# Performance work log

Hardware: AMD Instinct MI355X
Metric: run time of the kernel (lower is better)

Reference implementation:

```python
import jax, jax.numpy as jnp
import numpy as np

BIG = 1.0e9   # sentinel for masked distances / masked max
K_NBR = 64    # max_num_neighbors in radius()


def _fps(pos, n_sample):
    """Farthest point sampling on a single cloud pos [N, D] -> int32 [n_sample]."""
    n = pos.shape[0]

    def body(i, st):
        d, idxs = st
        last = pos[idxs[i - 1]]                              # [D]
        d = jnp.minimum(d, jnp.sum((pos - last) ** 2, axis=-1))
        return d, idxs.at[i].set(jnp.argmax(d).astype(jnp.int32))

    d0 = jnp.full((n,), BIG, pos.dtype)
    idxs0 = jnp.zeros((n_sample,), jnp.int32)
    _, idxs = jax.lax.fori_loop(1, n_sample, body, (d0, idxs0))
    return idxs


def _mlp2(h, w1, b1, w2, b2):
    # PyG MLP([a,b,c]) in eval mode (dropout off, batch-norm at default running
    # stats == identity): Linear -> ReLU -> Linear (plain last layer).
    return jax.nn.relu(h @ w1 + b1) @ w2 + b2


_gather = jax.vmap(lambda a, i: a[i])  # per-cloud fancy gather


def _sa(x, pos, ratio, r, w1, b1, w2, b2):
    """SAModule: FPS -> radius neighbors (<=K) -> PointConv (gather, MLP on
    [x_j, pos_j - pos_i], max-aggregate). Dense batched: x [B,N,C], pos [B,N,D]."""
    B, N, D = pos.shape
    M = int(round(N * ratio))
    idx = jax.vmap(lambda p: _fps(p, M))(pos)                 # [B, M]
    pos_q = _gather(pos, idx)                                 # [B, M, D]
    # pairwise squared distances query -> all points  [B, M, N]
    d2 = jnp.sum((pos_q[:, :, None, :] - pos[:, None, :, :]) ** 2, axis=-1)
    neg = jnp.where(d2 <= r * r, -d2, -BIG)
    vals, nbr = jax.lax.top_k(neg, K_NBR)                     # [B, M, K]
    valid = vals > -0.5 * BIG                                 # in-radius mask
    x_j = _gather(x, nbr)                                     # [B, M, K, C]
    rel = _gather(pos, nbr) - pos_q[:, :, None, :]            # [B, M, K, D]
    h = _mlp2(jnp.concatenate([x_j, rel], axis=-1), w1, b1, w2, b2)
    h = jnp.where(valid[..., None], h, -BIG)
    return jnp.max(h, axis=2), pos_q                          # max aggregation


def setup_inputs() -> dict:
    key = jax.random.key(0)
    ks = jax.random.split(key, 12)
    B, N, D, F = 8, 4096, 2, 5

    def lin(k, fi, fo):
        return (jax.random.normal(k, (fi, fo), jnp.float32) / np.sqrt(fi)).astype(jnp.float32)

    return {
        "x": jax.random.normal(ks[0], (B, N, F), jnp.float32),
        "pos": jax.random.uniform(ks[1], (B, N, D), jnp.float32),
        # sa1: MLP([5+2, 32, 64])
        "w1a": lin(ks[2], 7, 32),   "b1a": jnp.zeros((32,), jnp.float32),
        "w1b": lin(ks[3], 32, 64),  "b1b": jnp.zeros((64,), jnp.float32),
        # sa2: MLP([64+2, 64, 128])
        "w2a": lin(ks[4], 66, 64),  "b2a": jnp.zeros((64,), jnp.float32),
        "w2b": lin(ks[5], 64, 128), "b2b": jnp.zeros((128,), jnp.float32),
        # sa3 (global): MLP([128+2, 128, 256])
        "w3a": lin(ks[6], 130, 128), "b3a": jnp.zeros((128,), jnp.float32),
        "w3b": lin(ks[7], 128, 256), "b3b": jnp.zeros((256,), jnp.float32),
        # head: MLP([256, 256, 1024], norm=None)
        "w4a": lin(ks[8], 256, 256),  "b4a": jnp.zeros((256,), jnp.float32),
        "w4b": lin(ks[9], 256, 1024), "b4b": jnp.zeros((1024,), jnp.float32),
    }


def reference(x, pos, w1a, b1a, w1b, b1b, w2a, b2a, w2b, b2b,
              w3a, b3a, w3b, b3b, w4a, b4a, w4b, b4b):
    h1, p1 = _sa(x, pos, 0.5, 0.2, w1a, b1a, w1b, b1b)       # [B, N/2, 64]
    h2, p2 = _sa(h1, p1, 0.25, 0.4, w2a, b2a, w2b, b2b)      # [B, N/8, 128]
    g = _mlp2(jnp.concatenate([h2, p2], axis=-1), w3a, b3a, w3b, b3b)
    g = jnp.max(g, axis=1)                                    # global max pool [B, 256]
    return _mlp2(g, w4a, b4a, w4b, b4b)                       # [B, 1024]
```

## Files before the change

kernel.cpp:

```cpp
#include <hip/hip_runtime.h>
#include <hip/hip_cooperative_groups.h>

namespace cg = cooperative_groups;


#define DPP_UMAX(u, ctrl)                                                      \
  do {                                                                         \
    unsigned _o = (unsigned)__builtin_amdgcn_update_dpp(0, (int)(u), (ctrl),   \
                                                        0xf, 0xf, true);       \
    (u) = ((u) > _o) ? (u) : _o;                                               \
  } while (0)

template<int PPT, int T>
__device__ __forceinline__ void fps_stage(
    float (&xr)[PPT], float (&yr)[PPT], int Msel, int t,
    const float* srcx, const float* srcy,
    float* outx, float* outy,
    unsigned long long* sp ) {
  constexpr int NW = T / 64;
  constexpr int HP = PPT / 2;
  float lx = srcx[0], ly = srcy[0];
  if (t == 0) { outx[0] = lx; outy[0] = ly; }
  float d[PPT];
#pragma unroll
  for (int k = 0; k < PPT; ++k) d[k] = 1e9f;

  for (int i = 1; i < Msel; ++i) {
#pragma unroll
    for (int k = 0; k < PPT; ++k) {
      float dx = xr[k] - lx, dy = yr[k] - ly;
      float dd = __fadd_rn(__fmul_rn(dx, dx), __fmul_rn(dy, dy));
      d[k] = fminf(d[k], dd);
    }
    float bvA = d[0]; int bkA = 0;
    float bvB = d[HP]; int bkB = HP;
#pragma unroll
    for (int k = 1; k < HP; ++k) {
      if (d[k] > bvA)      { bvA = d[k];      bkA = k; }
      if (d[HP + k] > bvB) { bvB = d[HP + k]; bkB = HP + k; }
    }
    float bv = bvA; int bk = bkA;
    if (bvB > bvA) { bv = bvB; bk = bkB; }
    const int bp = t * PPT + bk;
    const unsigned mybits = __float_as_uint(bv);
    unsigned u = mybits;
    DPP_UMAX(u, 0x111);
    DPP_UMAX(u, 0x112);
    DPP_UMAX(u, 0x114);
    DPP_UMAX(u, 0x118);
    DPP_UMAX(u, 0x142);
    DPP_UMAX(u, 0x143);
    const unsigned wvb = (unsigned)__builtin_amdgcn_readlane((int)u, 63);
    const unsigned long long tmask = __ballot(mybits == wvb);
    const int fl = (int)__builtin_ctzll(tmask);
    const int wbp = __builtin_amdgcn_readlane(bp, fl);
    const int par = i & 1;
    if ((t & 63) == 0)
      sp[par * NW + (t >> 6)] =
          ((unsigned long long)wvb << 32) | (unsigned)(~wbp);
    __syncthreads();
    const unsigned long long* sl = &sp[par * NW];
    unsigned long long best = sl[0];
#pragma unroll
    for (int j = 1; j < NW; ++j) {
      unsigned long long v = sl[j];
      best = (v > best) ? v : best;
    }
    const int wi = (int)(~(unsigned)best);
    lx = srcx[wi]; ly = srcy[wi];
    if (t == 0) { outx[i] = lx; outy[i] = ly; }
  }
}

__global__ __launch_bounds__(512) void mega_kernel(
    const float* __restrict__ pos,
    const float* __restrict__ xin,
    float* __restrict__ posq1,
    float* __restrict__ posq2,
    float* __restrict__ h1,
    const float* __restrict__ W1, const float* __restrict__ B1,
    const float* __restrict__ W2, const float* __restrict__ B2)
{
  constexpr int N = 4096, M1 = 2048, M2 = 512, T = 512;
  constexpr int PPT = N / T, PPT2 = M1 / T, NW = T / 64;
  constexpr int H = 32, CI2 = 7, HS = 36, W1P = 8;
  __shared__ union {
    struct {
      float sx[N], sy[N];
      float wlx[M1], wly[M1];
      float wl2x[M2], wl2y[M2];
      unsigned long long sp[2 * NW];
    } f;
    struct {
      float sW1t[H * W1P];
      float sB1[H];
      float sHH[8 * 64 * HS];
      int   sNbr[8][64];
    } c;
  } sh;
  const int bid = blockIdx.x, t = threadIdx.x;
  cg::grid_group grid = cg::this_grid();

  float xr[PPT], yr[PPT];
  if (bid < 8) {
    const int b = bid;
    const float4* p4 =
        (const float4*)(pos + (size_t)b * N * 2 + (size_t)t * PPT * 2);
#pragma unroll
    for (int q = 0; q < PPT / 2; ++q) {
      float4 v = p4[q];
      xr[2 * q + 0] = v.x; yr[2 * q + 0] = v.y;
      xr[2 * q + 1] = v.z; yr[2 * q + 1] = v.w;
    }
#pragma unroll
    for (int k = 0; k < PPT; ++k) {
      int pt = t * PPT + k;
      sh.f.sx[pt] = xr[k]; sh.f.sy[pt] = yr[k];
    }
    __syncthreads();
    fps_stage<PPT, T>(xr, yr, M1, t, sh.f.sx, sh.f.sy, sh.f.wlx, sh.f.wly,
                      sh.f.sp);
    __syncthreads();
    for (int j = t; j < M1; j += T)
      ((float2*)posq1)[(size_t)b * M1 + j] =
          make_float2(sh.f.wlx[j], sh.f.wly[j]);
    __threadfence();
  }
  grid.sync();

  if (bid < 8) {
    const int b = bid;
    float x2[PPT2], y2[PPT2];
#pragma unroll
    for (int k = 0; k < PPT2; ++k) {
      x2[k] = sh.f.wlx[t * PPT2 + k];
      y2[k] = sh.f.wly[t * PPT2 + k];
    }
    fps_stage<PPT2, T>(x2, y2, M2, t, sh.f.wlx, sh.f.wly, sh.f.wl2x, sh.f.wl2y,
                       sh.f.sp);
    __syncthreads();
    for (int j = t; j < M2; j += T)
      ((float2*)posq2)[(size_t)b * M2 + j] =
          make_float2(sh.f.wl2x[j], sh.f.wl2y[j]);
  } else {
    for (int j = t; j < CI2 * H; j += T) {
      int cc = j / H, hh = j - cc * H;
      sh.c.sW1t[hh * W1P + cc] = W1[j];
    }
    for (int j = t; j < H; j += T) sh.c.sB1[j] = B1[j];
    __syncthreads();
    const int wv = t >> 6, lane = t & 63;
    const unsigned long long below = (1ULL << lane) - 1ULL;
    float* hbase = &sh.c.sHH[wv * 64 * HS];
    int* snb = sh.c.sNbr[wv];
    for (int wid = (bid - 8) * 8 + wv; wid < 16384; wid += 248 * 8) {
      const int b = wid >> 11;
      const float qx = posq1[2 * wid + 0], qy = posq1[2 * wid + 1];
      const float* p = pos + (size_t)b * N * 2;
      snb[lane] = -1;
      unsigned bits[64];
      int cnt = 0;
#pragma unroll
      for (int k = 0; k < 64; ++k) {
        int pt = lane + (k << 6);
        float dx = p[pt * 2 + 0] - qx, dy = p[pt * 2 + 1] - qy;
        float dd = __fadd_rn(__fmul_rn(dx, dx), __fmul_rn(dy, dy));
        bool inr = (dd <= 0.04f);
        bits[k] = inr ? __float_as_uint(dd) : 0xFFFFFFFFu;
        cnt += __popcll(__ballot(inr));
      }
      if (cnt <= 64) {
        int base = 0;
#pragma unroll
        for (int k = 0; k < 64; ++k) {
          bool s = (bits[k] != 0xFFFFFFFFu);
          unsigned long long m = __ballot(s);
          if (s) snb[base + __popcll(m & below)] = lane + (k << 6);
          base += __popcll(m);
        }
      } else {
        unsigned lo = 0, hi = __float_as_uint(0.04f);
        while (lo < hi) {
          unsigned mid = lo + ((hi - lo) >> 1);
          int c = 0;
#pragma unroll
          for (int k = 0; k < 64; ++k) c += __popcll(__ballot(bits[k] <= mid));
          if (c >= 64) hi = mid; else lo = mid + 1;
        }
        int cless = 0;
#pragma unroll
        for (int k = 0; k < 64; ++k) cless += __popcll(__ballot(bits[k] < lo));
        const int need = 64 - cless;
        int base = 0, tiecnt = 0;
#pragma unroll
        for (int k = 0; k < 64; ++k) {
          bool tie = (bits[k] == lo);
          unsigned long long tm = __ballot(tie);
          bool s = (bits[k] < lo) ||
                   (tie && (tiecnt + __popcll(tm & below)) < need);
          tiecnt += __popcll(tm);
          unsigned long long m = __ballot(s);
          if (s) snb[base + __popcll(m & below)] = lane + (k << 6);
          base += __popcll(m);
        }
      }
      const int idx = snb[lane];
      const unsigned long long vm = __ballot(idx >= 0);
      const int ii = (idx < 0) ? 0 : idx;
      float in[CI2];
      {
        const float* xp = xin + ((size_t)b * N + ii) * 5;
#pragma unroll
        for (int c = 0; c < 5; ++c) in[c] = xp[c];
        const float* pp = p + (size_t)ii * 2;
        in[5] = pp[0] - qx;
        in[6] = pp[1] - qy;
      }
#pragma unroll
      for (int h = 0; h < H; h += 4) {
        float vv[4];
#pragma unroll
        for (int j = 0; j < 4; ++j) {
          float a = sh.c.sB1[h + j];
#pragma unroll
          for (int c = 0; c < CI2; ++c)
            a = fmaf(in[c], sh.c.sW1t[(h + j) * W1P + c], a);
          vv[j] = fmaxf(a, 0.0f);
        }
        *(float4*)&hbase[lane * HS + h] = make_float4(vv[0], vv[1], vv[2], vv[3]);
      }
      const int o = lane;
      float w2r[H];
#pragma unroll
      for (int h = 0; h < H; ++h) w2r[h] = W2[h * 64 + o];
      const float b2o = B2[o];
      float m = -1e30f;
      for (int n = 0; n < 64; ++n) {
        const float4* hp = (const float4*)&hbase[n * HS];
        float a = b2o;
#pragma unroll
        for (int j = 0; j < H / 4; ++j) {
          float4 hv = hp[j];
          a = fmaf(hv.x, w2r[4 * j + 0], a);
          a = fmaf(hv.y, w2r[4 * j + 1], a);
          a = fmaf(hv.z, w2r[4 * j + 2], a);
          a = fmaf(hv.w, w2r[4 * j + 3], a);
        }
        a = ((vm >> n) & 1ULL) ? a : -1e9f;
        m = fmaxf(m, a);
      }
      h1[(size_t)wid * 64 + o] = m;
    }
  }
}

template<int CPL>
__global__ __launch_bounds__(256) void nbr_kernel(
    const float* __restrict__ pts, const float* __restrict__ posq,
    int* __restrict__ nbr, int M, int NPTS, int total_q, float R2) {
  const int wid = blockIdx.x * 4 + (threadIdx.x >> 6);
  if (wid >= total_q) return;
  const int lane = threadIdx.x & 63;
  const int b = wid / M;
  const float qx = posq[(size_t)wid * 2 + 0], qy = posq[(size_t)wid * 2 + 1];
  const float* p = pts + (size_t)b * NPTS * 2;
  unsigned bits[CPL];
  int cnt = 0;
#pragma unroll
  for (int k = 0; k < CPL; ++k) {
    int pt = lane + (k << 6);
    float dx = p[pt * 2 + 0] - qx, dy = p[pt * 2 + 1] - qy;
    float dd = __fadd_rn(__fmul_rn(dx, dx), __fmul_rn(dy, dy));
    bool inr = (dd <= R2);
    bits[k] = inr ? __float_as_uint(dd) : 0xFFFFFFFFu;
    cnt += __popcll(__ballot(inr));
  }
  const unsigned long long below = (1ULL << lane) - 1ULL;
  if (cnt <= 64) {
    int base = 0;
#pragma unroll
    for (int k = 0; k < CPL; ++k) {
      bool s = (bits[k] != 0xFFFFFFFFu);
      unsigned long long m = __ballot(s);
      if (s) nbr[(size_t)wid * 64 + base + __popcll(m & below)] = lane + (k << 6);
      base += __popcll(m);
    }
    for (int j = base + lane; j < 64; j += 64) nbr[(size_t)wid * 64 + j] = -1;
  } else {
    unsigned lo = 0, hi = __float_as_uint(R2);
    while (lo < hi) {
      unsigned mid = lo + ((hi - lo) >> 1);
      int c = 0;
#pragma unroll
      for (int k = 0; k < CPL; ++k) c += __popcll(__ballot(bits[k] <= mid));
      if (c >= 64) hi = mid; else lo = mid + 1;
    }
    int cless = 0;
#pragma unroll
    for (int k = 0; k < CPL; ++k) cless += __popcll(__ballot(bits[k] < lo));
    const int need = 64 - cless;
    int base = 0, tiecnt = 0;
#pragma unroll
    for (int k = 0; k < CPL; ++k) {
      bool tie = (bits[k] == lo);
      unsigned long long tm = __ballot(tie);
      bool s = (bits[k] < lo) || (tie && (tiecnt + __popcll(tm & below)) < need);
      tiecnt += __popcll(tm);
      unsigned long long m = __ballot(s);
      if (s) nbr[(size_t)wid * 64 + base + __popcll(m & below)] = lane + (k << 6);
      base += __popcll(m);
    }
  }
}

template<int CIN, int H, int COUT, int QPB, int NPTS, int HS, int W1P>
__global__ __launch_bounds__(64 * QPB) void conv_kernel(
    const float* __restrict__ x, const float* __restrict__ pts,
    const float* __restrict__ posq, const int* __restrict__ nbr,
    const float* __restrict__ W1, const float* __restrict__ b1,
    const float* __restrict__ W2, const float* __restrict__ b2,
    float* __restrict__ out, int M) {
  constexpr int CI2 = CIN + 2;
  __shared__ float sW1t[H * W1P];
  __shared__ float sB1[H];
  __shared__ float sHH[QPB * 64 * HS];
  const int tid = threadIdx.x;
  for (int j = tid; j < CI2 * H; j += 64 * QPB) {
    int c = j / H, h = j - c * H;
    sW1t[h * W1P + c] = W1[j];
  }
  for (int j = tid; j < H; j += 64 * QPB) sB1[j] = b1[j];
  __syncthreads();
  const int wv = tid >> 6, lane = tid & 63;
  const int wid = blockIdx.x * QPB + wv;
  const int b = wid / M;
  const int idx = nbr[(size_t)wid * 64 + lane];
  const unsigned long long vm = __ballot(idx >= 0);
  const int ii = (idx < 0) ? 0 : idx;
  float in[CI2];
  {
    const float* xp = x + ((size_t)b * NPTS + ii) * CIN;
#pragma unroll
    for (int c = 0; c < CIN; ++c) in[c] = xp[c];
    float qx = posq[(size_t)wid * 2 + 0], qy = posq[(size_t)wid * 2 + 1];
    const float* pp = pts + ((size_t)b * NPTS + ii) * 2;
    in[CIN] = pp[0] - qx;
    in[CIN + 1] = pp[1] - qy;
  }
  float* hbase = &sHH[wv * 64 * HS];
#pragma unroll
  for (int h = 0; h < H; h += 4) {
    float vv[4];
#pragma unroll
    for (int j = 0; j < 4; ++j) {
      float a = sB1[h + j];
#pragma unroll
      for (int c = 0; c < CI2; ++c) a = fmaf(in[c], sW1t[(h + j) * W1P + c], a);
      vv[j] = fmaxf(a, 0.0f);
    }
    *(float4*)&hbase[lane * HS + h] = make_float4(vv[0], vv[1], vv[2], vv[3]);
  }
#pragma unroll
  for (int half = 0; half < COUT / 64; ++half) {
    const int o = half * 64 + lane;
    float w2r[H];
#pragma unroll
    for (int h = 0; h < H; ++h) w2r[h] = W2[h * COUT + o];
    const float b2o = b2[o];
    float m = -1e30f;
    for (int n = 0; n < 64; ++n) {
      const float4* hp = (const float4*)&hbase[n * HS];
      float a = b2o;
#pragma unroll
      for (int j = 0; j < H / 4; ++j) {
        float4 hv = hp[j];
        a = fmaf(hv.x, w2r[4 * j + 0], a);
        a = fmaf(hv.y, w2r[4 * j + 1], a);
        a = fmaf(hv.z, w2r[4 * j + 2], a);
        a = fmaf(hv.w, w2r[4 * j + 3], a);
      }
      a = ((vm >> n) & 1ULL) ? a : -1e9f;
      m = fmaxf(m, a);
    }
    out[(size_t)wid * COUT + o] = m;
  }
}

__global__ __launch_bounds__(256) void u_kernel(
    const float* __restrict__ h2, const float* __restrict__ posq2,
    const float* __restrict__ W3a, const float* __restrict__ b3a,
    float* __restrict__ u) {
  const int p = blockIdx.x * 2 + (threadIdx.x >> 7);
  const int h = threadIdx.x & 127;
  const float* hp = h2 + (size_t)p * 128;
  float a = b3a[h];
  for (int c = 0; c < 128; ++c) a = fmaf(hp[c], W3a[c * 128 + h], a);
  a = fmaf(posq2[(size_t)p * 2 + 0], W3a[128 * 128 + h], a);
  a = fmaf(posq2[(size_t)p * 2 + 1], W3a[129 * 128 + h], a);
  u[(size_t)p * 128 + h] = fmaxf(a, 0.0f);
}

__global__ __launch_bounds__(256) void g_kernel(
    const float* __restrict__ u, const float* __restrict__ W3b,
    const float* __restrict__ b3b, float* __restrict__ part) {
  __shared__ float su[64 * 128];
  const int bb = blockIdx.x;
  const float* up = u + (size_t)bb * 64 * 128;
  for (int j = threadIdx.x; j < 64 * 128; j += 256) su[j] = up[j];
  __syncthreads();
  const int o = threadIdx.x;
  float w[128];
#pragma unroll
  for (int h = 0; h < 128; ++h) w[h] = W3b[h * 256 + o];
  float m = -1e30f;
  for (int p = 0; p < 64; ++p) {
    float a = b3b[o];
    const float4* sp = (const float4*)&su[p * 128];
#pragma unroll
    for (int j = 0; j < 32; ++j) {
      float4 v = sp[j];
      a = fmaf(v.x, w[4 * j + 0], a);
      a = fmaf(v.y, w[4 * j + 1], a);
      a = fmaf(v.z, w[4 * j + 2], a);
      a = fmaf(v.w, w[4 * j + 3], a);
    }
    m = fmaxf(m, a);
  }
  part[(size_t)bb * 256 + o] = m;
}

__global__ __launch_bounds__(256) void head_kernel(
    const float* __restrict__ part, const float* __restrict__ W4a,
    const float* __restrict__ b4a, const float* __restrict__ W4b,
    const float* __restrict__ b4b, float* __restrict__ out) {
  __shared__ float g[256], h4[256];
  const int b = blockIdx.x, t = threadIdx.x;
  float m = part[(size_t)(b * 8 + 0) * 256 + t];
  for (int c = 1; c < 8; ++c) m = fmaxf(m, part[(size_t)(b * 8 + c) * 256 + t]);
  g[t] = m;
  __syncthreads();
  float a = b4a[t];
  for (int c = 0; c < 256; ++c) a = fmaf(g[c], W4a[c * 256 + t], a);
  h4[t] = fmaxf(a, 0.0f);
  __syncthreads();
  for (int jj = 0; jj < 4; ++jj) {
    int o = t + jj * 256;
    float a2 = b4b[o];
    for (int c = 0; c < 256; ++c) a2 = fmaf(h4[c], W4b[c * 1024 + o], a2);
    out[(size_t)b * 1024 + o] = a2;
  }
}

extern "C" void kernel_launch(void* const* d_in, const int* in_sizes, int n_in,
                              void* d_out, int out_size, void* d_ws, size_t ws_size,
                              hipStream_t stream) {
  (void)in_sizes; (void)n_in; (void)out_size; (void)ws_size;
  const float* x   = (const float*)d_in[0];
  const float* pos = (const float*)d_in[1];
  const float* w1a = (const float*)d_in[2];  const float* b1a = (const float*)d_in[3];
  const float* w1b = (const float*)d_in[4];  const float* b1b = (const float*)d_in[5];
  const float* w2a = (const float*)d_in[6];  const float* b2a = (const float*)d_in[7];
  const float* w2b = (const float*)d_in[8];  const float* b2b = (const float*)d_in[9];
  const float* w3a = (const float*)d_in[10]; const float* b3a = (const float*)d_in[11];
  const float* w3b = (const float*)d_in[12]; const float* b3b = (const float*)d_in[13];
  const float* w4a = (const float*)d_in[14]; const float* b4a = (const float*)d_in[15];
  const float* w4b = (const float*)d_in[16]; const float* b4b = (const float*)d_in[17];
  float* outp = (float*)d_out;

  char* ws = (char*)d_ws;
  size_t off = 0;
  float* posq1 = (float*)(ws + off); off += (size_t)8 * 2048 * 2 * 4;
  float* posq2 = (float*)(ws + off); off += (size_t)8 * 512 * 2 * 4;
  int*   nbr2  = (int*)  (ws + off); off += (size_t)4096 * 64 * 4;
  float* h1    = (float*)(ws + off); off += (size_t)16384 * 64 * 4;
  float* h2    = (float*)(ws + off); off += (size_t)4096 * 128 * 4;
  float* u3    = (float*)(ws + off); off += (size_t)4096 * 128 * 4;
  float* part  = (float*)(ws + off); off += (size_t)64 * 256 * 4;

  void* kargs[] = {(void*)&pos, (void*)&x, (void*)&posq1, (void*)&posq2,
                   (void*)&h1, (void*)&w1a, (void*)&b1a, (void*)&w1b,
                   (void*)&b1b};
  hipLaunchCooperativeKernel((void*)mega_kernel, dim3(256), dim3(512), kargs,
                             0, stream);
  nbr_kernel<32><<<dim3(1024), dim3(256), 0, stream>>>(posq1, posq2, nbr2,
                                                       512, 2048, 4096, 0.16f);
  conv_kernel<64, 64, 128, 2, 2048, 68, 68><<<dim3(2048), dim3(128), 0, stream>>>(
      h1, posq1, posq2, nbr2, w2a, b2a, w2b, b2b, h2, 512);
  u_kernel<<<dim3(2048), dim3(256), 0, stream>>>(h2, posq2, w3a, b3a, u3);
  g_kernel<<<dim3(64), dim3(256), 0, stream>>>(u3, w3b, b3b, part);
  head_kernel<<<dim3(8), dim3(256), 0, stream>>>(part, w4a, b4a, w4b, b4b, outp);
}
```

Measured before the change: 2.001 ms.

## Stream FPS results to overlap SA1 conv and fuse all stages into one cooperative kernel

The first FPS stage now publishes sampled points to global memory in chunks of 64, each followed by a per-cloud progress counter. The SA1 conv blocks spin on that counter, so they can start before FPS finishes instead of waiting on a grid barrier. The SA2 neighbor search and conv, the SA3 MLP with global max, and the head MLP all move into the same cooperative kernel, separated by grid syncs. This removes five extra kernel launches and the nbr2/u3 intermediate buffers. It also folds W2 register loads out of the per-query loop and adds a launch_bounds occupancy hint of one block. The risks are spin-wait overhead, correctness of the acquire/release fences, and later stages running on only 256 blocks at low occupancy.

```diff
diff --git a/kernel.cpp b/kernel.cpp
--- a/kernel.cpp
+++ b/kernel.cpp
@@ -11,16 +11,18 @@
     (u) = ((u) > _o) ? (u) : _o;                                               \
   } while (0)
 
-template<int PPT, int T>
+template<int PPT, int T, bool PUB>
 __device__ __forceinline__ void fps_stage(
     float (&xr)[PPT], float (&yr)[PPT], int Msel, int t,
     const float* srcx, const float* srcy,
     float* outx, float* outy,
-    unsigned long long* sp ) {
+    unsigned long long* sp ,
+    float2* pq1g, unsigned* prog) {
   constexpr int NW = T / 64;
   constexpr int HP = PPT / 2;
   float lx = srcx[0], ly = srcy[0];
   if (t == 0) { outx[0] = lx; outy[0] = ly; }
+  float px = lx, py = ly;
   float d[PPT];
 #pragma unroll
   for (int k = 0; k < PPT; ++k) d[k] = 1e9f;
@@ -69,41 +71,73 @@
     const int wi = (int)(~(unsigned)best);
     lx = srcx[wi]; ly = srcy[wi];
     if (t == 0) { outx[i] = lx; outy[i] = ly; }
+    if constexpr (PUB) {
+      if ((t >> 6) == NW - 1) {
+        const int lj = t & 63;
+        if (lj == (i & 63)) { px = lx; py = ly; }
+        if ((i & 63) == 63) {
+          pq1g[(i - 63) + lj] = make_float2(px, py);
+          __builtin_amdgcn_fence(__ATOMIC_RELEASE, "agent");
+          if (lj == 0)
+            __hip_atomic_store(prog, (unsigned)(i + 1), __ATOMIC_RELAXED,
+                               __HIP_MEMORY_SCOPE_AGENT);
+        }
+      }
+    }
   }
 }
 
-__global__ __launch_bounds__(512) void mega_kernel(
+union SharedU {
+  struct {
+    float sx[4096], sy[4096];
+    float wlx[2048], wly[2048];
+    float wl2x[512], wl2y[512];
+    unsigned long long sp[16];
+  } f;
+  struct {
+    float sW1t[32 * 8]; float sB1[32];
+    float sHH[8 * 64 * 36]; int sNbr[8][64];
+  } c1;
+  struct {
+    float sW1t[64 * 68]; float sB1[64];
+    float sHH[8 * 64 * 68]; int sNbr[8][64];
+  } c2;
+  struct { float su[16 * 128]; } g;
+  struct { float gg[256]; float h4[256]; } h;
+};
+
+__global__ __launch_bounds__(512, 1) void mega_kernel(
     const float* __restrict__ pos,
     const float* __restrict__ xin,
     float* __restrict__ posq1,
     float* __restrict__ posq2,
     float* __restrict__ h1,
-    const float* __restrict__ W1, const float* __restrict__ B1,
-    const float* __restrict__ W2, const float* __restrict__ B2)
-{
+    float* __restrict__ h2,
+    float* __restrict__ part,
+    unsigned* __restrict__ prog,
+    const float* __restrict__ w1a, const float* __restrict__ b1a,
+    const float* __restrict__ w1b, const float* __restrict__ b1b,
+    const float* __restrict__ w2a, const float* __restrict__ b2a,
+    const float* __restrict__ w2b, const float* __restrict__ b2b,
+    const float* __restrict__ w3a, const float* __restrict__ b3a,
+    const float* __restrict__ w3b, const float* __restrict__ b3b,
+    const float* __restrict__ w4a, const float* __restrict__ b4a,
+    const float* __restrict__ w4b, const float* __restrict__ b4b,
+    float* __restrict__ outp) {
   constexpr int N = 4096, M1 = 2048, M2 = 512, T = 512;
-  constexpr int PPT = N / T, PPT2 = M1 / T, NW = T / 64;
-  constexpr int H = 32, CI2 = 7, HS = 36, W1P = 8;
-  __shared__ union {
-    struct {
-      float sx[N], sy[N];
-      float wlx[M1], wly[M1];
-      float wl2x[M2], wl2y[M2];
-      unsigned long long sp[2 * NW];
-    } f;
-    struct {
-      float sW1t[H * W1P];
-      float sB1[H];
-      float sHH[8 * 64 * HS];
-      int   sNbr[8][64];
-    } c;
-  } sh;
+  constexpr int PPT = N / T, PPT2 = M1 / T;
+  __shared__ SharedU sh;
   const int bid = blockIdx.x, t = threadIdx.x;
   cg::grid_group grid = cg::this_grid();
 
-  float xr[PPT], yr[PPT];
+  if (bid < 8 && t == 0)
+    __hip_atomic_store(&prog[bid], 0u, __ATOMIC_RELAXED,
+                       __HIP_MEMORY_SCOPE_AGENT);
+  grid.sync();
+
   if (bid < 8) {
     const int b = bid;
+    float xr[PPT], yr[PPT];
     const float4* p4 =
         (const float4*)(pos + (size_t)b * N * 2 + (size_t)t * PPT * 2);
 #pragma unroll
@@ -118,44 +152,49 @@
       sh.f.sx[pt] = xr[k]; sh.f.sy[pt] = yr[k];
     }
     __syncthreads();
-    fps_stage<PPT, T>(xr, yr, M1, t, sh.f.sx, sh.f.sy, sh.f.wlx, sh.f.wly,
-                      sh.f.sp);
-    __syncthreads();
-    for (int j = t; j < M1; j += T)
-      ((float2*)posq1)[(size_t)b * M1 + j] =
-          make_float2(sh.f.wlx[j], sh.f.wly[j]);
-    __threadfence();
-  }
-  grid.sync();
-
-  if (bid < 8) {
-    const int b = bid;
+    fps_stage<PPT, T, true>(xr, yr, M1, t, sh.f.sx, sh.f.sy, sh.f.wlx,
+                            sh.f.wly, sh.f.sp,
+                            (float2*)posq1 + (size_t)b * M1, &prog[b]);
+    __syncthreads();
     float x2[PPT2], y2[PPT2];
 #pragma unroll
     for (int k = 0; k < PPT2; ++k) {
       x2[k] = sh.f.wlx[t * PPT2 + k];
       y2[k] = sh.f.wly[t * PPT2 + k];
     }
-    fps_stage<PPT2, T>(x2, y2, M2, t, sh.f.wlx, sh.f.wly, sh.f.wl2x, sh.f.wl2y,
-                       sh.f.sp);
+    fps_stage<PPT2, T, false>(x2, y2, M2, t, sh.f.wlx, sh.f.wly, sh.f.wl2x,
+                              sh.f.wl2y, sh.f.sp, nullptr, nullptr);
     __syncthreads();
     for (int j = t; j < M2; j += T)
       ((float2*)posq2)[(size_t)b * M2 + j] =
           make_float2(sh.f.wl2x[j], sh.f.wl2y[j]);
+    __builtin_amdgcn_fence(__ATOMIC_RELEASE, "agent");
   } else {
-    for (int j = t; j < CI2 * H; j += T) {
-      int cc = j / H, hh = j - cc * H;
-      sh.c.sW1t[hh * W1P + cc] = W1[j];
-    }
-    for (int j = t; j < H; j += T) sh.c.sB1[j] = B1[j];
+    for (int j = t; j < 7 * 32; j += T) {
+      int cc = j >> 5, hh = j & 31;
+      sh.c1.sW1t[hh * 8 + cc] = w1a[j];
+    }
+    if (t < 32) sh.c1.sB1[t] = b1a[t];
     __syncthreads();
     const int wv = t >> 6, lane = t & 63;
     const unsigned long long below = (1ULL << lane) - 1ULL;
-    float* hbase = &sh.c.sHH[wv * 64 * HS];
-    int* snb = sh.c.sNbr[wv];
-    for (int wid = (bid - 8) * 8 + wv; wid < 16384; wid += 248 * 8) {
-      const int b = wid >> 11;
-      const float qx = posq1[2 * wid + 0], qy = posq1[2 * wid + 1];
+    float* hbase = &sh.c1.sHH[wv * 64 * 36];
+    int* snb = sh.c1.sNbr[wv];
+    float w2r[32];
+#pragma unroll
+    for (int hh = 0; hh < 32; ++hh) w2r[hh] = w1b[hh * 64 + lane];
+    const float b2o = b1b[lane];
+    for (int wid = (bid - 8) * 8 + wv; wid < 16384; wid += 1984) {
+      const int b = wid >> 11, j = wid & 2047;
+      while (__hip_atomic_load(&prog[b], __ATOMIC_RELAXED,
+                               __HIP_MEMORY_SCOPE_AGENT) <= (unsigned)j)
+        __builtin_amdgcn_s_sleep(2);
+      __builtin_amdgcn_fence(__ATOMIC_ACQUIRE, "agent");
+      const unsigned long long pk = __hip_atomic_load(
+          (const unsigned long long*)(posq1 + 2 * (size_t)wid),
+          __ATOMIC_RELAXED, __HIP_MEMORY_SCOPE_AGENT);
+      const float qx = __uint_as_float((unsigned)pk);
+      const float qy = __uint_as_float((unsigned)(pk >> 32));
       const float* p = pos + (size_t)b * N * 2;
       snb[lane] = -1;
       unsigned bits[64];
@@ -207,7 +246,7 @@
       const int idx = snb[lane];
       const unsigned long long vm = __ballot(idx >= 0);
       const int ii = (idx < 0) ? 0 : idx;
-      float in[CI2];
+      float in[7];
       {
         const float* xp = xin + ((size_t)b * N + ii) * 5;
 #pragma unroll
@@ -217,237 +256,224 @@
         in[6] = pp[1] - qy;
       }
 #pragma unroll
-      for (int h = 0; h < H; h += 4) {
+      for (int hh = 0; hh < 32; hh += 4) {
         float vv[4];
 #pragma unroll
-        for (int j = 0; j < 4; ++j) {
-          float a = sh.c.sB1[h + j];
-#pragma unroll
-          for (int c = 0; c < CI2; ++c)
-            a = fmaf(in[c], sh.c.sW1t[(h + j) * W1P + c], a);
-          vv[j] = fmaxf(a, 0.0f);
-        }
-        *(float4*)&hbase[lane * HS + h] = make_float4(vv[0], vv[1], vv[2], vv[3]);
-      }
-      const int o = lane;
-      float w2r[H];
-#pragma unroll
-      for (int h = 0; h < H; ++h) w2r[h] = W2[h * 64 + o];
-      const float b2o = B2[o];
+        for (int jj = 0; jj < 4; ++jj) {
+          float a = sh.c1.sB1[hh + jj];
+#pragma unroll
+          for (int c = 0; c < 7; ++c)
+            a = fmaf(in[c], sh.c1.sW1t[(hh + jj) * 8 + c], a);
+          vv[jj] = fmaxf(a, 0.0f);
+        }
+        *(float4*)&hbase[lane * 36 + hh] =
+            make_float4(vv[0], vv[1], vv[2], vv[3]);
+      }
       float m = -1e30f;
       for (int n = 0; n < 64; ++n) {
-        const float4* hp = (const float4*)&hbase[n * HS];
+        const float4* hp = (const float4*)&hbase[n * 36];
         float a = b2o;
 #pragma unroll
-        for (int j = 0; j < H / 4; ++j) {
-          float4 hv = hp[j];
-          a = fmaf(hv.x, w2r[4 * j + 0], a);
-          a = fmaf(hv.y, w2r[4 * j + 1], a);
-          a = fmaf(hv.z, w2r[4 * j + 2], a);
-          a = fmaf(hv.w, w2r[4 * j + 3], a);
+        for (int jj = 0; jj < 8; ++jj) {
+          float4 hv = hp[jj];
+          a = fmaf(hv.x, w2r[4 * jj + 0], a);
+          a = fmaf(hv.y, w2r[4 * jj + 1], a);
+          a = fmaf(hv.z, w2r[4 * jj + 2], a);
+          a = fmaf(hv.w, w2r[4 * jj + 3], a);
         }
         a = ((vm >> n) & 1ULL) ? a : -1e9f;
         m = fmaxf(m, a);
       }
-      h1[(size_t)wid * 64 + o] = m;
-    }
+      h1[(size_t)wid * 64 + lane] = m;
+    }
+    __builtin_amdgcn_fence(__ATOMIC_RELEASE, "agent");
   }
-}
-
-template<int CPL>
-__global__ __launch_bounds__(256) void nbr_kernel(
-    const float* __restrict__ pts, const float* __restrict__ posq,
-    int* __restrict__ nbr, int M, int NPTS, int total_q, float R2) {
-  const int wid = blockIdx.x * 4 + (threadIdx.x >> 6);
-  if (wid >= total_q) return;
-  const int lane = threadIdx.x & 63;
-  const int b = wid / M;
-  const float qx = posq[(size_t)wid * 2 + 0], qy = posq[(size_t)wid * 2 + 1];
-  const float* p = pts + (size_t)b * NPTS * 2;
-  unsigned bits[CPL];
-  int cnt = 0;
-#pragma unroll
-  for (int k = 0; k < CPL; ++k) {
-    int pt = lane + (k << 6);
-    float dx = p[pt * 2 + 0] - qx, dy = p[pt * 2 + 1] - qy;
-    float dd = __fadd_rn(__fmul_rn(dx, dx), __fmul_rn(dy, dy));
-    bool inr = (dd <= R2);
-    bits[k] = inr ? __float_as_uint(dd) : 0xFFFFFFFFu;
-    cnt += __popcll(__ballot(inr));
+  __syncthreads();
+  grid.sync();
+  __builtin_amdgcn_fence(__ATOMIC_ACQUIRE, "agent");
+
+  {
+    for (int j = t; j < 66 * 64; j += T) {
+      int cc = j >> 6, hh = j & 63;
+      sh.c2.sW1t[hh * 68 + cc] = w2a[j];
+    }
+    if (t < 64) sh.c2.sB1[t] = b2a[t];
+    __syncthreads();
+    const int wv = t >> 6, lane = t & 63;
+    const unsigned long long below = (1ULL << lane) - 1ULL;
+    float* hb = &sh.c2.sHH[wv * 64 * 68];
+    int* snb = sh.c2.sNbr[wv];
+    for (int q = bid * 8 + wv; q < 4096; q += 2048) {
+      const int b = q >> 9;
+      const float qx = posq2[2 * (size_t)q], qy = posq2[2 * (size_t)q + 1];
+      const float* p = posq1 + (size_t)b * 2048 * 2;
+      snb[lane] = -1;
+      unsigned bits[32];
+      int cnt = 0;
+#pragma unroll
+      for (int k = 0; k < 32; ++k) {
+        int pt = lane + (k << 6);
+        float dx = p[pt * 2 + 0] - qx, dy = p[pt * 2 + 1] - qy;
+        float dd = __fadd_rn(__fmul_rn(dx, dx), __fmul_rn(dy, dy));
+        bool inr = (dd <= 0.16f);
+        bits[k] = inr ? __float_as_uint(dd) : 0xFFFFFFFFu;
+        cnt += __popcll(__ballot(inr));
+      }
+      if (cnt <= 64) {
+        int base = 0;
+#pragma unroll
+        for (int k = 0; k < 32; ++k) {
+          bool s = (bits[k] != 0xFFFFFFFFu);
+          unsigned long long m = __ballot(s);
+          if (s) snb[base + __popcll(m & below)] = lane + (k << 6);
+          base += __popcll(m);
+        }
+      } else {
+        unsigned lo = 0, hi = __float_as_uint(0.16f);
+        while (lo < hi) {
+          unsigned mid = lo + ((hi - lo) >> 1);
+          int c = 0;
+#pragma unroll
+          for (int k = 0; k < 32; ++k) c += __popcll(__ballot(bits[k] <= mid));
+          if (c >= 64) hi = mid; else lo = mid + 1;
+        }
+        int cless = 0;
+#pragma unroll
+        for (int k = 0; k < 32; ++k) cless += __popcll(__ballot(bits[k] < lo));
+        const int need = 64 - cless;
+        int base = 0, tiecnt = 0;
+#pragma unroll
+        for (int k = 0; k < 32; ++k) {
+          bool tie = (bits[k] == lo);
+          unsigned long long tm = __ballot(tie);
+          bool s = (bits[k] < lo) ||
+                   (tie && (tiecnt + __popcll(tm & below)) < need);
+          tiecnt += __popcll(tm);
+          unsigned long long m = __ballot(s);
+          if (s) snb[base + __popcll(m & below)] = lane + (k << 6);
+          base += __popcll(m);
+        }
+      }
+      const int idx = snb[lane];
+      const unsigned long long vm = __ballot(idx >= 0);
+      const int ii = (idx < 0) ? 0 : idx;
+      float in[66];
+      {
+        const float* xp = h1 + ((size_t)b * 2048 + ii) * 64;
+#pragma unroll
+        for (int c = 0; c < 64; ++c) in[c] = xp[c];
+        in[64] = p[ii * 2 + 0] - qx;
+        in[65] = p[ii * 2 + 1] - qy;
+      }
+#pragma unroll
+      for (int hh = 0; hh < 64; hh += 4) {
+        float vv[4];
+#pragma unroll
+        for (int jj = 0; jj < 4; ++jj) {
+          float a = sh.c2.sB1[hh + jj];
+#pragma unroll
+          for (int c = 0; c < 66; ++c)
+            a = fmaf(in[c], sh.c2.sW1t[(hh + jj) * 68 + c], a);
+          vv[jj] = fmaxf(a, 0.0f);
+        }
+        *(float4*)&hb[lane * 68 + hh] = make_float4(vv[0], vv[1], vv[2], vv[3]);
+      }
+#pragma unroll
+      for (int half = 0; half < 2; ++half) {
+        const int o = half * 64 + lane;
+        float w2r[64];
+#pragma unroll
+        for (int hh = 0; hh < 64; ++hh) w2r[hh] = w2b[hh * 128 + o];
+        const float b2o = b2b[o];
+        float m = -1e30f;
+        for (int n = 0; n < 64; ++n) {
+          const float4* hp = (const float4*)&hb[n * 68];
+          float a = b2o;
+#pragma unroll
+          for (int jj = 0; jj < 16; ++jj) {
+            float4 hv = hp[jj];
+            a = fmaf(hv.x, w2r[4 * jj + 0], a);
+            a = fmaf(hv.y, w2r[4 * jj + 1], a);
+            a = fmaf(hv.z, w2r[4 * jj + 2], a);
+            a = fmaf(hv.w, w2r[4 * jj + 3], a);
+          }
+          a = ((vm >> n) & 1ULL) ? a : -1e9f;
+          m = fmaxf(m, a);
+        }
+        h2[(size_t)q * 128 + o] = m;
+      }
+    }
+    __builtin_amdgcn_fence(__ATOMIC_RELEASE, "agent");
   }
-  const unsigned long long below = (1ULL << lane) - 1ULL;
-  if (cnt <= 64) {
-    int base = 0;
-#pragma unroll
-    for (int k = 0; k < CPL; ++k) {
-      bool s = (bits[k] != 0xFFFFFFFFu);
-      unsigned long long m = __ballot(s);
-      if (s) nbr[(size_t)wid * 64 + base + __popcll(m & below)] = lane + (k << 6);
-      base += __popcll(m);
-    }
-    for (int j = base + lane; j < 64; j += 64) nbr[(size_t)wid * 64 + j] = -1;
-  } else {
-    unsigned lo = 0, hi = __float_as_uint(R2);
-    while (lo < hi) {
-      unsigned mid = lo + ((hi - lo) >> 1);
-      int c = 0;
-#pragma unroll
-      for (int k = 0; k < CPL; ++k) c += __popcll(__ballot(bits[k] <= mid));
-      if (c >= 64) hi = mid; else lo = mid + 1;
-    }
-    int cless = 0;
-#pragma unroll
-    for (int k = 0; k < CPL; ++k) cless += __popcll(__ballot(bits[k] < lo));
-    const int need = 64 - cless;
-    int base = 0, tiecnt = 0;
-#pragma unroll
-    for (int k = 0; k < CPL; ++k) {
-      bool tie = (bits[k] == lo);
-      unsigned long long tm = __ballot(tie);
-      bool s = (bits[k] < lo) || (tie && (tiecnt + __popcll(tm & below)) < need);
-      tiecnt += __popcll(tm);
-      unsigned long long m = __ballot(s);
-      if (s) nbr[(size_t)wid * 64 + base + __popcll(m & below)] = lane + (k << 6);
-      base += __popcll(m);
-    }
+  __syncthreads();
+  grid.sync();
+  __builtin_amdgcn_fence(__ATOMIC_ACQUIRE, "agent");
+
+  {
+    const int p0 = bid * 16;
+#pragma unroll
+    for (int r = 0; r < 4; ++r) {
+      const int pl = (t >> 7) + r * 4;
+      const int hh = t & 127;
+      const int p = p0 + pl;
+      const float* hp = h2 + (size_t)p * 128;
+      float a = b3a[hh];
+      for (int c = 0; c < 128; ++c) a = fmaf(hp[c], w3a[c * 128 + hh], a);
+      a = fmaf(posq2[2 * (size_t)p + 0], w3a[128 * 128 + hh], a);
+      a = fmaf(posq2[2 * (size_t)p + 1], w3a[129 * 128 + hh], a);
+      sh.g.su[pl * 128 + hh] = fmaxf(a, 0.0f);
+    }
+    __syncthreads();
+    if (t < 256) {
+      const int o = t;
+      float w[128];
+#pragma unroll
+      for (int hh = 0; hh < 128; ++hh) w[hh] = w3b[hh * 256 + o];
+      float m = -1e30f;
+      for (int pp = 0; pp < 16; ++pp) {
+        float a = b3b[o];
+        const float4* sp4 = (const float4*)&sh.g.su[pp * 128];
+#pragma unroll
+        for (int jj = 0; jj < 32; ++jj) {
+          float4 v = sp4[jj];
+          a = fmaf(v.x, w[4 * jj + 0], a);
+          a = fmaf(v.y, w[4 * jj + 1], a);
+          a = fmaf(v.z, w[4 * jj + 2], a);
+          a = fmaf(v.w, w[4 * jj + 3], a);
+        }
+        m = fmaxf(m, a);
+      }
+      part[(size_t)bid * 256 + o] = m;
+    }
+    __builtin_amdgcn_fence(__ATOMIC_RELEASE, "agent");
   }
-}
-
-template<int CIN, int H, int COUT, int QPB, int NPTS, int HS, int W1P>
-__global__ __launch_bounds__(64 * QPB) void conv_kernel(
-    const float* __restrict__ x, const float* __restrict__ pts,
-    const float* __restrict__ posq, const int* __restrict__ nbr,
-    const float* __restrict__ W1, const float* __restrict__ b1,
-    const float* __restrict__ W2, const float* __restrict__ b2,
-    float* __restrict__ out, int M) {
-  constexpr int CI2 = CIN + 2;
-  __shared__ float sW1t[H * W1P];
-  __shared__ float sB1[H];
-  __shared__ float sHH[QPB * 64 * HS];
-  const int tid = threadIdx.x;
-  for (int j = tid; j < CI2 * H; j += 64 * QPB) {
-    int c = j / H, h = j - c * H;
-    sW1t[h * W1P + c] = W1[j];
-  }
-  for (int j = tid; j < H; j += 64 * QPB) sB1[j] = b1[j];
   __syncthreads();
-  const int wv = tid >> 6, lane = tid & 63;
-  const int wid = blockIdx.x * QPB + wv;
-  const int b = wid / M;
-  const int idx = nbr[(size_t)wid * 64 + lane];
-  const unsigned long long vm = __ballot(idx >= 0);
-  const int ii = (idx < 0) ? 0 : idx;
-  float in[CI2];
-  {
-    const float* xp = x + ((size_t)b * NPTS + ii) * CIN;
-#pragma unroll
-    for (int c = 0; c < CIN; ++c) in[c] = xp[c];
-    float qx = posq[(size_t)wid * 2 + 0], qy = posq[(size_t)wid * 2 + 1];
-    const float* pp = pts + ((size_t)b * NPTS + ii) * 2;
-    in[CIN] = pp[0] - qx;
-    in[CIN + 1] = pp[1] - qy;
-  }
-  float* hbase = &sHH[wv * 64 * HS];
-#pragma unroll
-  for (int h = 0; h < H; h += 4) {
-    float vv[4];
-#pragma unroll
-    for (int j = 0; j < 4; ++j) {
-      float a = sB1[h + j];
-#pragma unroll
-      for (int c = 0; c < CI2; ++c) a = fmaf(in[c], sW1t[(h + j) * W1P + c], a);
-      vv[j] = fmaxf(a, 0.0f);
-    }
-    *(float4*)&hbase[lane * HS + h] = make_float4(vv[0], vv[1], vv[2], vv[3]);
-  }
-#pragma unroll
-  for (int half = 0; half < COUT / 64; ++half) {
-    const int o = half * 64 + lane;
-    float w2r[H];
-#pragma unroll
-    for (int h = 0; h < H; ++h) w2r[h] = W2[h * COUT + o];
-    const float b2o = b2[o];
-    float m = -1e30f;
-    for (int n = 0; n < 64; ++n) {
-      const float4* hp = (const float4*)&hbase[n * HS];
-      float a = b2o;
-#pragma unroll
-      for (int j = 0; j < H / 4; ++j) {
-        float4 hv = hp[j];
-        a = fmaf(hv.x, w2r[4 * j + 0], a);
-        a = fmaf(hv.y, w2r[4 * j + 1], a);
-        a = fmaf(hv.z, w2r[4 * j + 2], a);
-        a = fmaf(hv.w, w2r[4 * j + 3], a);
-      }
-      a = ((vm >> n) & 1ULL) ? a : -1e9f;
-      m = fmaxf(m, a);
-    }
-    out[(size_t)wid * COUT + o] = m;
-  }
-}
-
-__global__ __launch_bounds__(256) void u_kernel(
-    const float* __restrict__ h2, const float* __restrict__ posq2,
-    const float* __restrict__ W3a, const float* __restrict__ b3a,
-    float* __restrict__ u) {
-  const int p = blockIdx.x * 2 + (threadIdx.x >> 7);
-  const int h = threadIdx.x & 127;
-  const float* hp = h2 + (size_t)p * 128;
-  float a = b3a[h];
-  for (int c = 0; c < 128; ++c) a = fmaf(hp[c], W3a[c * 128 + h], a);
-  a = fmaf(posq2[(size_t)p * 2 + 0], W3a[128 * 128 + h], a);
-  a = fmaf(posq2[(size_t)p * 2 + 1], W3a[129 * 128 + h], a);
-  u[(size_t)p * 128 + h] = fmaxf(a, 0.0f);
-}
-
-__global__ __launch_bounds__(256) void g_kernel(
-    const float* __restrict__ u, const float* __restrict__ W3b,
-    const float* __restrict__ b3b, float* __restrict__ part) {
-  __shared__ float su[64 * 128];
-  const int bb = blockIdx.x;
-  const float* up = u + (size_t)bb * 64 * 128;
-  for (int j = threadIdx.x; j < 64 * 128; j += 256) su[j] = up[j];
-  __syncthreads();
-  const int o = threadIdx.x;
-  float w[128];
-#pragma unroll
-  for (int h = 0; h < 128; ++h) w[h] = W3b[h * 256 + o];
-  float m = -1e30f;
-  for (int p = 0; p < 64; ++p) {
-    float a = b3b[o];
-    const float4* sp = (const float4*)&su[p * 128];
-#pragma unroll
-    for (int j = 0; j < 32; ++j) {
-      float4 v = sp[j];
-      a = fmaf(v.x, w[4 * j + 0], a);
-      a = fmaf(v.y, w[4 * j + 1], a);
-      a = fmaf(v.z, w[4 * j + 2], a);
-      a = fmaf(v.w, w[4 * j + 3], a);
-    }
-    m = fmaxf(m, a);
-  }
-  part[(size_t)bb * 256 + o] = m;
-}
-
-__global__ __launch_bounds__(256) void head_kernel(
-    const float* __restrict__ part, const float* __restrict__ W4a,
-    const float* __restrict__ b4a, const float* __restrict__ W4b,
-    const float* __restrict__ b4b, float* __restrict__ out) {
-  __shared__ float g[256], h4[256];
-  const int b = blockIdx.x, t = threadIdx.x;
-  float m = part[(size_t)(b * 8 + 0) * 256 + t];
-  for (int c = 1; c < 8; ++c) m = fmaxf(m, part[(size_t)(b * 8 + c) * 256 + t]);
-  g[t] = m;
-  __syncthreads();
-  float a = b4a[t];
-  for (int c = 0; c < 256; ++c) a = fmaf(g[c], W4a[c * 256 + t], a);
-  h4[t] = fmaxf(a, 0.0f);
-  __syncthreads();
-  for (int jj = 0; jj < 4; ++jj) {
-    int o = t + jj * 256;
-    float a2 = b4b[o];
-    for (int c = 0; c < 256; ++c) a2 = fmaf(h4[c], W4b[c * 1024 + o], a2);
-    out[(size_t)b * 1024 + o] = a2;
+  grid.sync();
+  __builtin_amdgcn_fence(__ATOMIC_ACQUIRE, "agent");
+
+  if (bid < 8) {
+    if (t < 256) {
+      float m = part[((size_t)bid * 32) * 256 + t];
+      for (int c = 1; c < 32; ++c)
+        m = fmaxf(m, part[((size_t)bid * 32 + c) * 256 + t]);
+      sh.h.gg[t] = m;
+    }
+    __syncthreads();
+    if (t < 256) {
+      float a = b4a[t];
+      for (int c = 0; c < 256; ++c) a = fmaf(sh.h.gg[c], w4a[c * 256 + t], a);
+      sh.h.h4[t] = fmaxf(a, 0.0f);
+    }
+    __syncthreads();
+    if (t < 256) {
+#pragma unroll
+      for (int jj = 0; jj < 4; ++jj) {
+        int o = t + jj * 256;
+        float a2 = b4b[o];
+        for (int c = 0; c < 256; ++c) a2 = fmaf(sh.h.h4[c], w4b[c * 1024 + o], a2);
+        outp[(size_t)bid * 1024 + o] = a2;
+      }
+    }
   }
 }
 
@@ -469,24 +495,21 @@
 
   char* ws = (char*)d_ws;
   size_t off = 0;
-  float* posq1 = (float*)(ws + off); off += (size_t)8 * 2048 * 2 * 4;
-  float* posq2 = (float*)(ws + off); off += (size_t)8 * 512 * 2 * 4;
-  int*   nbr2  = (int*)  (ws + off); off += (size_t)4096 * 64 * 4;
-  float* h1    = (float*)(ws + off); off += (size_t)16384 * 64 * 4;
-  float* h2    = (float*)(ws + off); off += (size_t)4096 * 128 * 4;
-  float* u3    = (float*)(ws + off); off += (size_t)4096 * 128 * 4;
-  float* part  = (float*)(ws + off); off += (size_t)64 * 256 * 4;
-
-  void* kargs[] = {(void*)&pos, (void*)&x, (void*)&posq1, (void*)&posq2,
-                   (void*)&h1, (void*)&w1a, (void*)&b1a, (void*)&w1b,
-                   (void*)&b1b};
+  float*    posq1 = (float*)(ws + off); off += (size_t)8 * 2048 * 2 * 4;
+  float*    posq2 = (float*)(ws + off); off += (size_t)8 * 512 * 2 * 4;
+  float*    h1    = (float*)(ws + off); off += (size_t)16384 * 64 * 4;
+  float*    h2    = (float*)(ws + off); off += (size_t)4096 * 128 * 4;
+  float*    part  = (float*)(ws + off); off += (size_t)256 * 256 * 4;
+  unsigned* prog  = (unsigned*)(ws + off); off += 8 * 4;
+
+  void* kargs[] = {
+      (void*)&pos, (void*)&x, (void*)&posq1, (void*)&posq2, (void*)&h1,
+      (void*)&h2, (void*)&part, (void*)&prog,
+      (void*)&w1a, (void*)&b1a, (void*)&w1b, (void*)&b1b,
+      (void*)&w2a, (void*)&b2a, (void*)&w2b, (void*)&b2b,
+      (void*)&w3a, (void*)&b3a, (void*)&w3b, (void*)&b3b,
+      (void*)&w4a, (void*)&b4a, (void*)&w4b, (void*)&b4b,
+      (void*)&outp};
   hipLaunchCooperativeKernel((void*)mega_kernel, dim3(256), dim3(512), kargs,
                              0, stream);
-  nbr_kernel<32><<<dim3(1024), dim3(256), 0, stream>>>(posq1, posq2, nbr2,
-                                                       512, 2048, 4096, 0.16f);
-  conv_kernel<64, 64, 128, 2, 2048, 68, 68><<<dim3(2048), dim3(128), 0, stream>>>(
-      h1, posq1, posq2, nbr2, w2a, b2a, w2b, b2b, h2, 512);
-  u_kernel<<<dim3(2048), dim3(256), 0, stream>>>(h2, posq2, w3a, b3a, u3);
-  g_kernel<<<dim3(64), dim3(256), 0, stream>>>(u3, w3b, b3b, part);
-  head_kernel<<<dim3(8), dim3(256), 0, stream>>>(part, w4a, b4a, w4b, b4b, outp);
 }
```

New measurement: 2.124 ms. +6.2%, slower.
